# Optimization experiments

Hardware: AMD Instinct MI355X
Metric: run time of the kernel (lower is better)

The kernel has to match this reference:

```python
import jax, jax.numpy as jnp
import numpy as np

H = 128; W = 128; HW = H * W
B = 4          # batch_size
D = 256        # feat_dim
HEADS = 8
HD = D // HEADS
S = 256        # num_slots_total
POS = 512      # num_pos_samples
NEG = 256      # num_neg_samples
NS = POS + NEG # num_samples
LN_EPS = 1e-5


def _layer_norm(x, axis=-1, eps=LN_EPS):
    mean = jnp.mean(x, axis=axis, keepdims=True)
    var = jnp.mean(jnp.square(x - mean), axis=axis, keepdims=True)
    return (x - mean) * jax.lax.rsqrt(var + eps)


def setup_inputs() -> dict:
    key = jax.random.key(0)
    ks = jax.random.split(key, 8)
    slots = jax.random.normal(ks[0], (1, S, D), jnp.float32)
    features = jax.random.normal(ks[1], (HW, B, D), jnp.float32)
    pos_encodings = jax.random.normal(ks[2], (HW, B, D), jnp.float32)
    curio_maps = jax.random.uniform(ks[3], (S, H, W), jnp.float32)
    batch_idx = jax.random.randint(ks[4], (S,), 0, B)
    scale = 1.0 / np.sqrt(D)
    in_proj_weight = jax.random.normal(ks[5], (3 * D, D), jnp.float32) * scale
    in_proj_bias = jnp.zeros((3 * D,), jnp.float32)
    out_proj_w = jax.random.normal(ks[6], (D, D), jnp.float32) * scale
    out_proj_b = jnp.zeros((D,), jnp.float32)
    ln_w = jnp.ones((D,), jnp.float32)
    ln_b = jnp.zeros((D,), jnp.float32)
    return {
        'slots': slots, 'features': features, 'pos_encodings': pos_encodings,
        'curio_maps': curio_maps, 'batch_idx': batch_idx,
        'in_proj_weight': in_proj_weight, 'in_proj_bias': in_proj_bias,
        'out_proj_w': out_proj_w, 'out_proj_b': out_proj_b,
        'ln_w': ln_w, 'ln_b': ln_b, 'max_mask_entries': 100,
    }


def reference(slots, features, pos_encodings, curio_maps, batch_idx,
              in_proj_weight, in_proj_bias, out_proj_w, out_proj_b,
              ln_w, ln_b, max_mask_entries):
    ns_total = slots.shape[1]
    # ---- sample(): curiosity-guided top-k sampling -------------------------
    flat = curio_maps.reshape(ns_total, -1)                 # [S, H*W]
    sorted_idx = jnp.argsort(-flat, axis=1)                 # descending
    pos_idx = sorted_idx[:, :POS]
    neg_pool = sorted_idx[:, POS:flat.shape[1] - max_mask_entries]
    # deterministic stand-in for random.sample over the negative pool
    neg_idx = neg_pool[:, :NEG]
    feat_idx = jnp.concatenate([pos_idx, neg_idx], axis=1).T  # [NS, S]

    # ---- update_slots(): gather + projected multi-head cross-attention -----
    bi = batch_idx[None, :]                                 # [1, S]
    f = features[feat_idx, bi, :]                           # [NS, S, D]
    p = pos_encodings[feat_idx, bi, :]                      # [NS, S, D]
    keys = f + p
    values = f[:POS]                                        # [POS, S, D]

    Wq, Wk, Wv = in_proj_weight[:D], in_proj_weight[D:2 * D], in_proj_weight[2 * D:]
    bq, bk, bv = in_proj_bias[:D], in_proj_bias[D:2 * D], in_proj_bias[2 * D:]
    scaling = float(HD) ** -0.5
    q = (jnp.einsum('bsd,ed->bse', slots, Wq) + bq) * scaling   # [1, S, D]
    k = jnp.einsum('nsd,ed->nse', keys, Wk) + bk                # [NS, S, D]
    v = jnp.einsum('nsd,ed->nse', values, Wv) + bv              # [POS, S, D]

    q = q.reshape(ns_total * HEADS, 1, HD)                      # [S*h, 1, hd]
    k = k.reshape(NS, ns_total * HEADS, HD).transpose(1, 0, 2)  # [S*h, NS, hd]
    v = v.reshape(POS, ns_total * HEADS, HD).transpose(1, 0, 2) # [S*h, POS, hd]

    aff = jnp.einsum('nqd,nkd->nqk', q, k)                      # [S*h, 1, NS]
    attn = jax.nn.softmax(aff[:, :, :POS], axis=-1)
    out = jnp.einsum('nqk,nkd->nqd', attn, v)                   # [S*h, 1, hd]
    out = out.reshape(1, ns_total, D)
    out = jnp.einsum('bsd,ed->bse', out, out_proj_w) + out_proj_b

    slots_new = slots + out
    slots_new = _layer_norm(slots_new, axis=-1) * ln_w + ln_b   # [1, S, D]

    # normalized slot-feature affinities (head-averaged, per-slot layernorm)
    aff2 = aff.reshape(ns_total, HEADS, NS).transpose(2, 0, 1)  # [NS, S, h]
    aff2 = jnp.mean(aff2, axis=-1)                              # [NS, S]
    norm_aff = _layer_norm(aff2.T, axis=-1).T                   # [NS, S]
    norm_aff = jax.lax.stop_gradient(norm_aff)
    return slots_new, norm_aff
```

## Files before the change

### kernel.cpp

```cpp
#include <hip/hip_runtime.h>
#include <math.h>

#define NSLOT 256
#define HWN   16384
#define D_    256
#define BB    4
#define NSEL  768
#define NPOS  512
#define NHEAD 8
#define SEGS  20

typedef __attribute__((ext_vector_type(8))) short short8v;
typedef __attribute__((ext_vector_type(4))) float float4v;

#define GLD16(g, l)                                                        \
  __builtin_amdgcn_global_load_lds(                                        \
      (__attribute__((address_space(1))) void*)(g),                        \
      (__attribute__((address_space(3))) void*)(l), 16, 0, 0)

#define BFLO(u) __uint_as_float((u) << 16)
#define BFHI(u) __uint_as_float((u) & 0xffff0000u)

__device__ __forceinline__ unsigned short f2bf(float x) {
  unsigned u = __float_as_uint(x);
  unsigned r = u + 0x7fffu + ((u >> 16) & 1u);
  return (unsigned short)(r >> 16);
}
__device__ __forceinline__ unsigned int pk2(float a, float b) {
  return (unsigned)f2bf(a) | ((unsigned)f2bf(b) << 16);
}

union PrepSmem {
  struct {
    unsigned int hist[4096];
    unsigned int wsum[16];
    unsigned long long skey[SEGS * 64];
    int sBstar;
    unsigned int sCount;
  } tk;
  struct {
    float srow[4][D_];
    float qrow[4][D_];
    float qkl[4][NHEAD][D_];
    float qsl[4][D_];
  } qp;
};

__global__ __launch_bounds__(1024) void prep_kernel(
    const float* __restrict__ curio, int* __restrict__ feat_sel,
    const float* __restrict__ slots, const float* __restrict__ ipw,
    const float* __restrict__ ipb, float* __restrict__ qbk_g,
    unsigned short* __restrict__ qkb16,
    const float* __restrict__ fsrc, const float* __restrict__ psrc,
    unsigned short* __restrict__ kpf) {
  __shared__ PrepSmem sm;
  int B = blockIdx.x;
  int t = threadIdx.x;

  if (B < 256) {
    int s = B;
    int wave = t >> 6, lane = t & 63;
    const float* row = curio + (size_t)s * HWN;

    for (int i = t; i < 4096; i += 1024) sm.tk.hist[i] = 0;
    if (t == 0) sm.tk.sCount = 0;
    __syncthreads();
    for (int j = t; j < HWN; j += 1024) {
      unsigned int bits = __float_as_uint(row[j]);
      atomicAdd(&sm.tk.hist[bits >> 18], 1u);
    }
    __syncthreads();
    unsigned int cs = sm.tk.hist[t * 4] + sm.tk.hist[t * 4 + 1] +
                      sm.tk.hist[t * 4 + 2] + sm.tk.hist[t * 4 + 3];
    unsigned int v = cs;
#pragma unroll
    for (int off = 1; off < 64; off <<= 1) {
      unsigned int u = __shfl_down(v, off, 64);
      if (lane + off < 64) v += u;
    }
    if (lane == 0) sm.tk.wsum[wave] = v;
    __syncthreads();
    unsigned int above = 0;
    for (int w2 = wave + 1; w2 < 16; w2++) above += sm.tk.wsum[w2];
    unsigned int sufAfter = above + (v - cs);
    if (sufAfter < NSEL && sufAfter + cs >= NSEL) {
      unsigned int local = sufAfter;
      for (int b2 = t * 4 + 3; b2 >= t * 4; b2--) {
        unsigned int c = sm.tk.hist[b2];
        if (local + c >= NSEL) { sm.tk.sBstar = b2; break; }
        local += c;
      }
    }
    __syncthreads();
    int bstar = sm.tk.sBstar;
    for (int j = t; j < HWN; j += 1024) {
      unsigned int bits = __float_as_uint(row[j]);
      bool cand = ((int)(bits >> 18) >= bstar);
      unsigned long long mask = __ballot(cand);
      unsigned int base = 0;
      int lcnt = __popcll(mask);
      if (lane == 0 && lcnt) base = atomicAdd(&sm.tk.sCount, (unsigned)lcnt);
      base = __shfl(base, 0, 64);
      if (cand) {
        unsigned pos = base + __popcll(mask & ((1ull << lane) - 1ull));
        if (pos < SEGS * 64)
          sm.tk.skey[pos] = ((unsigned long long)bits << 14) |
                            (unsigned long long)(16383 - j);
      }
    }
    __syncthreads();
    unsigned int M = sm.tk.sCount;
    if (M > SEGS * 64) M = SEGS * 64;
    for (int i = t; i < SEGS * 64; i += 1024) if (i >= (int)M) sm.tk.skey[i] = 0ull;
    __syncthreads();
    for (int seg = wave; seg < SEGS; seg += 16) {
      unsigned long long kv = sm.tk.skey[seg * 64 + lane];
#pragma unroll
      for (int k = 2; k <= 64; k <<= 1) {
#pragma unroll
        for (int j2 = k >> 1; j2 > 0; j2 >>= 1) {
          unsigned long long o = __shfl_xor(kv, j2, 64);
          bool lower = ((lane & j2) == 0);
          bool descblk = ((lane & k) == 0);
          bool wantmax = (descblk == lower);
          kv = (wantmax == (kv >= o)) ? kv : o;
        }
      }
      sm.tk.skey[seg * 64 + lane] = kv;
    }
    __syncthreads();
    for (int e = t; e < SEGS * 64; e += 1024) {
      unsigned long long key = sm.tk.skey[e];
      if (key == 0ull) continue;
      int seg = e >> 6;
      int rank = e & 63;
      for (int g = 0; g < SEGS; g++) {
        if (g == seg) continue;
        const unsigned long long* sp = &sm.tk.skey[g * 64];
        int lo = 0, hi = 64;
        while (lo < hi) {
          int mid = (lo + hi) >> 1;
          if (sp[mid] > key) lo = mid + 1; else hi = mid;
        }
        rank += lo;
      }
      if (rank < NSEL) feat_sel[s * NSEL + rank] = 16383 - (int)(key & 16383ull);
    }
  } else if (B < 320) {
    int sub = t >> 8, tt = t & 255;
    int s = (B - 256) * 4 + sub;
    float* srow = sm.qp.srow[sub];
    float* qrow = sm.qp.qrow[sub];
    float* qsl = sm.qp.qsl[sub];
    srow[tt] = slots[s * D_ + tt];
    __syncthreads();
    {
      const float* wq = ipw + (size_t)tt * D_;
      float acc = ipb[tt];
      for (int d = 0; d < D_; d++) acc += srow[d] * wq[d];
      qrow[tt] = acc * 0.17677669529663689f;
    }
    __syncthreads();
    float qsum = 0.f;
    for (int h = 0; h < NHEAD; h++) {
      const float* wkbase = ipw + (size_t)(D_ + h * 32) * D_ + tt;
      float a = 0.f;
      for (int e = 0; e < 32; e++) a += qrow[h * 32 + e] * wkbase[(size_t)e * D_];
      sm.qp.qkl[sub][h][tt] = a;
      qsum += a;
    }
    qsl[tt] = qsum;
    if (tt < NHEAD) {
      float a = 0.f;
      for (int e = 0; e < 32; e++) a += qrow[tt * 32 + e] * ipb[D_ + tt * 32 + e];
      qbk_g[s * NHEAD + tt] = a;
    }
    __syncthreads();
    for (int i = 0; i < 16; i++) {
      int e = tt * 16 + i;
      int kc = e >> 9, l = (e >> 3) & 63, j = e & 7;
      int cc = l & 15, k = kc * 32 + ((l >> 4) & 3) * 8 + j;
      float v = (cc < NHEAD) ? sm.qp.qkl[sub][cc][k] : ((cc == NHEAD) ? qsl[k] : 0.f);
      qkb16[(size_t)s * 4096 + e] = f2bf(v);
    }
  } else {
    int stride = 512 * 1024;
    for (int u = (B - 320) * 1024 + t; u < HWN * BB * 32; u += stride) {
      int row = u >> 5, b2 = u & 31;
      int c8 = b2 << 3;
      const float4* f4 = (const float4*)(fsrc + (size_t)row * D_ + c8);
      const float4* p4 = (const float4*)(psrc + (size_t)row * D_ + c8);
      float4 a0 = f4[0], a1 = f4[1], b0 = p4[0], b1 = p4[1];
      uint4 kp, ff;
      kp.x = pk2(a0.x + b0.x, a0.y + b0.y);
      kp.y = pk2(a0.z + b0.z, a0.w + b0.w);
      kp.z = pk2(a1.x + b1.x, a1.y + b1.y);
      kp.w = pk2(a1.z + b1.z, a1.w + b1.w);
      ff.x = pk2(a0.x, a0.y); ff.y = pk2(a0.z, a0.w);
      ff.z = pk2(a1.x, a1.y); ff.w = pk2(a1.z, a1.w);
      int sig = row & 7;
      *(uint4*)(kpf + (size_t)row * 512 + ((b2 ^ sig) << 3)) = kp;
      *(uint4*)(kpf + (size_t)row * 512 + 256 + c8) = ff;
    }
  }
}

__global__ __launch_bounds__(256, 3) void aff_pv_mfma_kernel(
    const unsigned short* __restrict__ kpf,
    const unsigned short* __restrict__ qkb16,
    const int* __restrict__ batch_idx, const int* __restrict__ feat_sel,
    const float* __restrict__ qbk_g,
    float* __restrict__ fbar_part,
    float* __restrict__ expsum_part,
    float* __restrict__ stat_part,
    float* __restrict__ aff2_g) {
  __shared__ unsigned short kplds[4][4096];
  __shared__ unsigned short qkb[4096];
  __shared__ float wlds[4][16][17];
  __shared__ float fbar[NHEAD][D_];
  __shared__ float a2buf[384];
  __shared__ int   sfsel[384];
  __shared__ float esums[4][NHEAD];
  __shared__ float sstat[4][2];
  __shared__ float qbkmean_s;

  int b = blockIdx.x, s = b >> 1, half = b & 1;
  int t = threadIdx.x, w = t >> 6, lane = t & 63;
  int bi = batch_idx[s];
  int col = lane & 15, quad = lane >> 4;

  {
    const uint4* src = (const uint4*)(qkb16 + (size_t)s * 4096);
    ((uint4*)qkb)[t] = src[t];
    ((uint4*)qkb)[t + 256] = src[t + 256];
  }
  for (int i = t; i < 384; i += 256) sfsel[i] = feat_sel[s * NSEL + half + 2 * i];
  for (int i = t; i < NHEAD * D_; i += 256) ((float*)fbar)[i] = 0.f;
  if (t == 0) {
    float m = 0.f;
    for (int h = 0; h < NHEAD; h++) m += qbk_g[s * NHEAD + h];
    qbkmean_s = m * 0.125f;
  }
  __syncthreads();

  unsigned short* kslot = &kplds[w][0];
  float acc[NHEAD][4];
#pragma unroll
  for (int h = 0; h < NHEAD; h++)
#pragma unroll
    for (int c = 0; c < 4; c++) acc[h][c] = 0.f;
  float esum_acc = 0.f;

  auto ISSUE_KP = [&](int L) {
#pragma unroll
    for (int p = 0; p < 8; p++) {
      int r0 = sfsel[L + 2 * p], r1 = sfsel[L + 2 * p + 1];
      unsigned ridx = (unsigned)((lane < 32 ? r0 : r1) * BB + bi);
      const unsigned short* src = kpf + (size_t)ridx * 512 + (lane & 31) * 8;
      GLD16(src, kslot + p * 512);
    }
  };

  ISSUE_KP(w * 64);
#pragma unroll 1
  for (int i = 0; i < 6; i++) {
    int L = (i < 4) ? (w * 64 + i * 16) : (256 + w * 32 + (i - 4) * 16);
    asm volatile("s_waitcnt vmcnt(0)" ::: "memory");
    bool pos = (i < 4);
    uint2 fu[16];
    if (pos) {
#pragma unroll
      for (int r = 0; r < 16; r++)
        fu[r] = *(const uint2*)(kpf + (size_t)((unsigned)sfsel[L + r] * BB + bi) * 512 +
                                256 + lane * 4);
    }
    unsigned sig = ((unsigned)sfsel[L + col] * BB + bi) & 7u;
    short8v afr[8];
#pragma unroll
    for (int kc = 0; kc < 8; kc++) {
      unsigned blk = ((unsigned)(kc * 4 + quad)) ^ sig;
      afr[kc] = *(const short8v*)(kslot + col * 256 + blk * 8);
    }
    asm volatile("s_waitcnt lgkmcnt(0)" ::: "memory");
    __builtin_amdgcn_sched_barrier(0);
    if (i < 5) {
      int Ln = (i < 3) ? (w * 64 + (i + 1) * 16) : (256 + w * 32 + (i - 3) * 16);
      ISSUE_KP(Ln);
    }
    float4v c = {0.f, 0.f, 0.f, 0.f};
#pragma unroll
    for (int kc = 0; kc < 8; kc++) {
      short8v bfr = *(const short8v*)&qkb[(kc * 64 + lane) * 8];
      c = __builtin_amdgcn_mfma_f32_16x16x32_bf16(afr[kc], bfr, c, 0, 0, 0);
    }
    if (pos) {
      if (col < NHEAD) {
        float e0 = __expf(c[0]), e1 = __expf(c[1]), e2 = __expf(c[2]), e3 = __expf(c[3]);
        esum_acc += e0 + e1 + e2 + e3;
        wlds[w][quad * 4 + 0][col] = e0;
        wlds[w][quad * 4 + 1][col] = e1;
        wlds[w][quad * 4 + 2][col] = e2;
        wlds[w][quad * 4 + 3][col] = e3;
      } else if (col == NHEAD) {
        float qm = qbkmean_s;
#pragma unroll
        for (int j = 0; j < 4; j++) a2buf[L + quad * 4 + j] = c[j] * 0.125f + qm;
      }
      asm volatile("s_waitcnt lgkmcnt(0)" ::: "memory");
      __builtin_amdgcn_sched_barrier(0);
#pragma unroll
      for (int r = 0; r < 16; r++) {
        const float4 w0 = *(const float4*)&wlds[w][r][0];
        const float4 w1 = *(const float4*)&wlds[w][r][4];
        float f0 = BFLO(fu[r].x), f1 = BFHI(fu[r].x), f2 = BFLO(fu[r].y), f3 = BFHI(fu[r].y);
        acc[0][0] += w0.x * f0; acc[0][1] += w0.x * f1; acc[0][2] += w0.x * f2; acc[0][3] += w0.x * f3;
        acc[1][0] += w0.y * f0; acc[1][1] += w0.y * f1; acc[1][2] += w0.y * f2; acc[1][3] += w0.y * f3;
        acc[2][0] += w0.z * f0; acc[2][1] += w0.z * f1; acc[2][2] += w0.z * f2; acc[2][3] += w0.z * f3;
        acc[3][0] += w0.w * f0; acc[3][1] += w0.w * f1; acc[3][2] += w0.w * f2; acc[3][3] += w0.w * f3;
        acc[4][0] += w1.x * f0; acc[4][1] += w1.x * f1; acc[4][2] += w1.x * f2; acc[4][3] += w1.x * f3;
        acc[5][0] += w1.y * f0; acc[5][1] += w1.y * f1; acc[5][2] += w1.y * f2; acc[5][3] += w1.y * f3;
        acc[6][0] += w1.z * f0; acc[6][1] += w1.z * f1; acc[6][2] += w1.z * f2; acc[6][3] += w1.z * f3;
        acc[7][0] += w1.w * f0; acc[7][1] += w1.w * f1; acc[7][2] += w1.w * f2; acc[7][3] += w1.w * f3;
      }
    } else {
      if (col == NHEAD) {
        float qm = qbkmean_s;
#pragma unroll
        for (int j = 0; j < 4; j++) a2buf[L + quad * 4 + j] = c[j] * 0.125f + qm;
      }
    }
  }

  esum_acc += __shfl_xor(esum_acc, 16, 64);
  esum_acc += __shfl_xor(esum_acc, 32, 64);
  if (lane < NHEAD) esums[w][lane] = esum_acc;
#pragma unroll
  for (int h = 0; h < NHEAD; h++) {
    atomicAdd(&fbar[h][lane * 4 + 0], acc[h][0]);
    atomicAdd(&fbar[h][lane * 4 + 1], acc[h][1]);
    atomicAdd(&fbar[h][lane * 4 + 2], acc[h][2]);
    atomicAdd(&fbar[h][lane * 4 + 3], acc[h][3]);
  }
  __syncthreads();

  {
    float v1 = a2buf[t];
    float v2 = (t < 128) ? a2buf[256 + t] : 0.f;
    float ls = v1 + v2, lq = v1 * v1 + v2 * v2;
#pragma unroll
    for (int off = 32; off >= 1; off >>= 1) { ls += __shfl_xor(ls, off, 64); lq += __shfl_xor(lq, off, 64); }
    if (lane == 0) { sstat[w][0] = ls; sstat[w][1] = lq; }
  }
  __syncthreads();
  if (t < NHEAD) {
    expsum_part[b * NHEAD + t] = esums[0][t] + esums[1][t] + esums[2][t] + esums[3][t];
  } else if (t == NHEAD) {
    stat_part[b * 2 + 0] = sstat[0][0] + sstat[1][0] + sstat[2][0] + sstat[3][0];
    stat_part[b * 2 + 1] = sstat[0][1] + sstat[1][1] + sstat[2][1] + sstat[3][1];
  }
  aff2_g[s * NSEL + half + 2 * t] = a2buf[t];
  if (t < 128) aff2_g[s * NSEL + half + 2 * (256 + t)] = a2buf[256 + t];
  ((float4*)(fbar_part + (size_t)b * 2048))[t] = ((float4*)fbar)[t];
  ((float4*)(fbar_part + (size_t)b * 2048))[t + 256] = ((float4*)fbar)[t + 256];
}

__global__ __launch_bounds__(1024) void finish_kernel(
    const float* __restrict__ slots,
    const float* __restrict__ expsum_part, const float* __restrict__ stat_part,
    const float* __restrict__ aff2_g, const float* __restrict__ fbar_part,
    const float* __restrict__ ipw, const float* __restrict__ ipb,
    const float* __restrict__ wout, const float* __restrict__ bout,
    const float* __restrict__ lnw, const float* __restrict__ lnb,
    float* __restrict__ slots_new, float* __restrict__ norm_aff) {
  __shared__ float fbar[NHEAD][D_];
  __shared__ float srow[D_];
  __shared__ float outv[D_];
  __shared__ float pq[1024];
  __shared__ float redS[4], redQ[4];
  int s = blockIdx.x, t = threadIdx.x, wave = t >> 6, lane = t & 63;

  float st0 = stat_part[s * 4 + 0] + stat_part[s * 4 + 2];
  float st1 = stat_part[s * 4 + 1] + stat_part[s * 4 + 3];
  float mean_a = st0 * (1.0f / NSEL);
  float var_a = st1 * (1.0f / NSEL) - mean_a * mean_a;
  float rstd_a = rsqrtf(var_a + 1e-5f);
  if (t < NSEL) norm_aff[(size_t)t * NSLOT + s] = (aff2_g[s * NSEL + t] - mean_a) * rstd_a;

  if (t < 512) {
    int h = t >> 6;
    float inv = 1.0f / (expsum_part[s * 16 + h] + expsum_part[s * 16 + 8 + h]);
    const float4 a = ((const float4*)(fbar_part + (size_t)s * 4096))[t];
    const float4 c = ((const float4*)(fbar_part + (size_t)s * 4096 + 2048))[t];
    float4 r;
    r.x = (a.x + c.x) * inv; r.y = (a.y + c.y) * inv;
    r.z = (a.z + c.z) * inv; r.w = (a.w + c.w) * inv;
    ((float4*)fbar)[t] = r;
  }
  if (t < 64) ((float4*)srow)[t] = ((const float4*)(slots + (size_t)s * D_))[t];
  __syncthreads();

  {
    int o = t >> 2, part = t & 3, h = o >> 5;
    const float4* wv = (const float4*)(ipw + (size_t)(2 * D_ + o) * D_ + part * 64);
    float a = 0.f;
#pragma unroll
    for (int i = 0; i < 16; i++) {
      float4 w = wv[i];
      int d = part * 64 + i * 4;
      a += fbar[h][d] * w.x + fbar[h][d + 1] * w.y + fbar[h][d + 2] * w.z + fbar[h][d + 3] * w.w;
    }
    pq[t] = a;
  }
  __syncthreads();
  if (t < D_)
    outv[t] = pq[t * 4] + pq[t * 4 + 1] + pq[t * 4 + 2] + pq[t * 4 + 3] + ipb[2 * D_ + t];
  __syncthreads();

  {
    int o = t >> 2, part = t & 3;
    const float4* w4 = (const float4*)(wout + (size_t)o * D_ + part * 64);
    float a = 0.f;
#pragma unroll
    for (int i = 0; i < 16; i++) {
      float4 w = w4[i];
      int d = part * 64 + i * 4;
      a += outv[d] * w.x + outv[d + 1] * w.y + outv[d + 2] * w.z + outv[d + 3] * w.w;
    }
    pq[t] = a;
  }
  __syncthreads();
  float v = 0.f;
  if (t < D_) {
    v = srow[t] + pq[t * 4] + pq[t * 4 + 1] + pq[t * 4 + 2] + pq[t * 4 + 3] + bout[t];
    float ls = v, lq = v * v;
#pragma unroll
    for (int off = 32; off >= 1; off >>= 1) { ls += __shfl_xor(ls, off, 64); lq += __shfl_xor(lq, off, 64); }
    if (lane == 0) { redS[wave] = ls; redQ[wave] = lq; }
  }
  __syncthreads();
  if (t < D_) {
    float tots = redS[0] + redS[1] + redS[2] + redS[3];
    float totq = redQ[0] + redQ[1] + redQ[2] + redQ[3];
    float mean = tots * (1.0f / D_);
    float var = totq * (1.0f / D_) - mean * mean;
    float rstd = rsqrtf(var + 1e-5f);
    slots_new[s * D_ + t] = (v - mean) * rstd * lnw[t] + lnb[t];
  }
}

extern "C" void kernel_launch(void* const* d_in, const int* in_sizes, int n_in,
                              void* d_out, int out_size, void* d_ws, size_t ws_size,
                              hipStream_t stream) {
  const float* slots    = (const float*)d_in[0];
  const float* features = (const float*)d_in[1];
  const float* posenc   = (const float*)d_in[2];
  const float* curio    = (const float*)d_in[3];
  const int*   batch_idx= (const int*)d_in[4];
  const float* ipw      = (const float*)d_in[5];
  const float* ipb      = (const float*)d_in[6];
  const float* wout     = (const float*)d_in[7];
  const float* bout     = (const float*)d_in[8];
  const float* lnw      = (const float*)d_in[9];
  const float* lnb      = (const float*)d_in[10];

  char* ws = (char*)d_ws;
  size_t off = 0;
  int*   feat_sel    = (int*)(ws + off);   off += 256 * 768 * 4;
  float* qbk_g       = (float*)(ws + off); off += 256 * 8 * 4;
  unsigned short* qkb16 = (unsigned short*)(ws + off); off += 256 * 4096 * 2;
  float* fbar_part   = (float*)(ws + off); off += 256 * 2 * 8 * 256 * 4;
  float* expsum_part = (float*)(ws + off); off += 256 * 2 * 8 * 4;
  float* stat_part   = (float*)(ws + off); off += 256 * 2 * 2 * 4;
  float* aff2_g      = (float*)(ws + off); off += 256 * 768 * 4;
  size_t kpf_off = (off + 1023) & ~(size_t)1023;
  unsigned short* kpf = (unsigned short*)(ws + kpf_off);

  float* out_f = (float*)d_out;

  prep_kernel<<<832, 1024, 0, stream>>>(curio, feat_sel, slots, ipw, ipb,
                                        qbk_g, qkb16, features, posenc, kpf);
  aff_pv_mfma_kernel<<<NSLOT * 2, 256, 0, stream>>>(kpf, qkb16, batch_idx, feat_sel,
                                                    qbk_g, fbar_part, expsum_part,
                                                    stat_part, aff2_g);
  finish_kernel<<<NSLOT, 1024, 0, stream>>>(slots, expsum_part, stat_part, aff2_g,
                                            fbar_part, ipw, ipb, wout, bout, lnw, lnb,
                                            out_f, out_f + 65536);
}
```

Measured before the change: 137.5 us.

## Fold per-slot query projection into top-k blocks and shrink prep grid

The separate query-projection blocks (64 blocks, 4 slots each) are removed. Each top-k block now computes its own slot's q and q·Wk projection with all 1024 threads after the selection finishes, using float4 weight loads and a 4-way split reduction. The feature/posenc conversion branch drops from 512 to 256 blocks and gets a 2x unroll. This cuts the grid from 832 to 512 blocks, so the work is spread differently across CUs. In exchange the top-k blocks get longer and the bulk conversion has fewer blocks to hide memory latency.

```diff
diff --git a/kernel.cpp b/kernel.cpp
--- a/kernel.cpp
+++ b/kernel.cpp
@@ -39,10 +39,11 @@
     unsigned int sCount;
   } tk;
   struct {
-    float srow[4][D_];
-    float qrow[4][D_];
-    float qkl[4][NHEAD][D_];
-    float qsl[4][D_];
+    float srow[D_];
+    float qrow[D_];
+    float qkl[NHEAD][D_];
+    float qsl[D_];
+    float pq[1024];
   } qp;
 };
 
@@ -146,46 +147,59 @@
       }
       if (rank < NSEL) feat_sel[s * NSEL + rank] = 16383 - (int)(key & 16383ull);
     }
-  } else if (B < 320) {
-    int sub = t >> 8, tt = t & 255;
-    int s = (B - 256) * 4 + sub;
-    float* srow = sm.qp.srow[sub];
-    float* qrow = sm.qp.qrow[sub];
-    float* qsl = sm.qp.qsl[sub];
-    srow[tt] = slots[s * D_ + tt];
+    __syncthreads();
+
+    if (t < 256) sm.qp.srow[t] = slots[s * D_ + t];
     __syncthreads();
     {
-      const float* wq = ipw + (size_t)tt * D_;
-      float acc = ipb[tt];
-      for (int d = 0; d < D_; d++) acc += srow[d] * wq[d];
-      qrow[tt] = acc * 0.17677669529663689f;
-    }
-    __syncthreads();
-    float qsum = 0.f;
-    for (int h = 0; h < NHEAD; h++) {
-      const float* wkbase = ipw + (size_t)(D_ + h * 32) * D_ + tt;
+      int o = t >> 2, part = t & 3;
+      const float4* w4 = (const float4*)(ipw + (size_t)o * D_ + part * 64);
       float a = 0.f;
-      for (int e = 0; e < 32; e++) a += qrow[h * 32 + e] * wkbase[(size_t)e * D_];
-      sm.qp.qkl[sub][h][tt] = a;
-      qsum += a;
-    }
-    qsl[tt] = qsum;
-    if (tt < NHEAD) {
+#pragma unroll
+      for (int i = 0; i < 16; i++) {
+        float4 w = w4[i];
+        int d = part * 64 + i * 4;
+        a += sm.qp.srow[d] * w.x + sm.qp.srow[d + 1] * w.y +
+             sm.qp.srow[d + 2] * w.z + sm.qp.srow[d + 3] * w.w;
+      }
+      sm.qp.pq[t] = a;
+    }
+    __syncthreads();
+    if (t < 256)
+      sm.qp.qrow[t] = (sm.qp.pq[t * 4] + sm.qp.pq[t * 4 + 1] + sm.qp.pq[t * 4 + 2] +
+                       sm.qp.pq[t * 4 + 3] + ipb[t]) * 0.17677669529663689f;
+    __syncthreads();
+    for (int e = t; e < 2048; e += 1024) {
+      int h = e >> 8, c = e & 255;
+      const float* wk = ipw + (size_t)(D_ + h * 32) * D_ + c;
       float a = 0.f;
-      for (int e = 0; e < 32; e++) a += qrow[tt * 32 + e] * ipb[D_ + tt * 32 + e];
-      qbk_g[s * NHEAD + tt] = a;
-    }
-    __syncthreads();
-    for (int i = 0; i < 16; i++) {
-      int e = tt * 16 + i;
+#pragma unroll
+      for (int k = 0; k < 32; k++) a += sm.qp.qrow[h * 32 + k] * wk[(size_t)k * D_];
+      sm.qp.qkl[h][c] = a;
+    }
+    __syncthreads();
+    if (t < 256) {
+      float qs = 0.f;
+#pragma unroll
+      for (int h = 0; h < NHEAD; h++) qs += sm.qp.qkl[h][t];
+      sm.qp.qsl[t] = qs;
+    }
+    if (t < NHEAD) {
+      float a = 0.f;
+      for (int e = 0; e < 32; e++) a += sm.qp.qrow[t * 32 + e] * ipb[D_ + t * 32 + e];
+      qbk_g[s * NHEAD + t] = a;
+    }
+    __syncthreads();
+    for (int e = t; e < 4096; e += 1024) {
       int kc = e >> 9, l = (e >> 3) & 63, j = e & 7;
       int cc = l & 15, k = kc * 32 + ((l >> 4) & 3) * 8 + j;
-      float v = (cc < NHEAD) ? sm.qp.qkl[sub][cc][k] : ((cc == NHEAD) ? qsl[k] : 0.f);
-      qkb16[(size_t)s * 4096 + e] = f2bf(v);
+      float v2 = (cc < NHEAD) ? sm.qp.qkl[cc][k] : ((cc == NHEAD) ? sm.qp.qsl[k] : 0.f);
+      qkb16[(size_t)s * 4096 + e] = f2bf(v2);
     }
   } else {
-    int stride = 512 * 1024;
-    for (int u = (B - 320) * 1024 + t; u < HWN * BB * 32; u += stride) {
+    int stride = 256 * 1024;
+#pragma unroll 2
+    for (int u = (B - 256) * 1024 + t; u < HWN * BB * 32; u += stride) {
       int row = u >> 5, b2 = u & 31;
       int c8 = b2 << 3;
       const float4* f4 = (const float4*)(fsrc + (size_t)row * D_ + c8);
@@ -477,7 +491,7 @@
 
   float* out_f = (float*)d_out;
 
-  prep_kernel<<<832, 1024, 0, stream>>>(curio, feat_sel, slots, ipw, ipb,
+  prep_kernel<<<512, 1024, 0, stream>>>(curio, feat_sel, slots, ipw, ipb,
                                         qbk_g, qkb16, features, posenc, kpf);
   aff_pv_mfma_kernel<<<NSLOT * 2, 256, 0, stream>>>(kpf, qkb16, batch_idx, feat_sel,
                                                     qbk_g, fbar_part, expsum_part,
```

After: 150.1 us. 1.09x slower.
